# Performance work log

Hardware: AMD Instinct MI355X
Metric: run time of the kernel (lower is better)

Reference implementation:

```python
import jax, jax.numpy as jnp
import numpy as np

B, T, HE, L, HD = 512, 512, 512, 64, 512

def setup_inputs() -> dict:
    key = jax.random.key(0)
    ks = jax.random.split(key, 16)
    def w(k, shape):
        return jax.random.normal(k, shape, dtype=jnp.float32) * 0.05
    z32 = lambda n: jnp.zeros((n,), jnp.float32)
    return {
        "input_tensor": jax.random.normal(ks[0], (B, T, 1), dtype=jnp.float32),
        # encoder LSTMCell (keras gate order i, f, g, o)
        "enc_W": w(ks[1], (1, 4 * HE)),
        "enc_U": w(ks[2], (HE, 4 * HE)),
        "enc_b": z32(4 * HE),
        # encoder mu / std heads
        "emu_W": w(ks[3], (HE, L)), "emu_b": z32(L),
        "estd_W": w(ks[4], (HE, L)), "estd_b": z32(L),
        # decoder first-state dense (tanh)
        "dfs_W": w(ks[5], (L, HD)), "dfs_b": z32(HD),
        # decoder LSTMCell
        "dec_W": w(ks[6], (L, 4 * HD)),
        "dec_U": w(ks[7], (HD, 4 * HD)),
        "dec_b": z32(4 * HD),
        # decoder mu / std heads (Dense(1))
        "dmu_W": w(ks[8], (HD, 1)), "dmu_b": z32(1),
        "dstd_W": w(ks[9], (HD, 1)), "dstd_b": z32(1),
    }

def _lstm_update(gates, c):
    i, f, g, o = jnp.split(gates, 4, axis=-1)
    c_new = jax.nn.sigmoid(f) * c + jax.nn.sigmoid(i) * jnp.tanh(g)
    h_new = jax.nn.sigmoid(o) * jnp.tanh(c_new)
    return h_new, c_new

def reference(input_tensor, enc_W, enc_U, enc_b, emu_W, emu_b, estd_W, estd_b,
              dfs_W, dfs_b, dec_W, dec_U, dec_b, dmu_W, dmu_b, dstd_W, dstd_b):
    x = input_tensor
    Bn, Tn = x.shape[0], x.shape[1]
    He = enc_U.shape[0]

    # ---- encoder: LSTM over time, keep final h ----
    def enc_step(carry, xt):
        h, c = carry
        gates = xt @ enc_W + h @ enc_U + enc_b
        return _lstm_update(gates, c), None
    h0 = jnp.zeros((Bn, He), x.dtype)
    (hT, _), _ = jax.lax.scan(enc_step, (h0, h0), jnp.swapaxes(x, 0, 1))

    mu_enc = hT @ emu_W + emu_b                       # [B, L]
    sigma_enc = jax.nn.softplus(hT @ estd_W + estd_b)  # [B, L]
    z = mu_enc  # call() uses reparam=False -> latent returns mu

    # ---- decoder: LSTM fed constant z each step ----
    hd = jnp.tanh(z @ dfs_W + dfs_b)                  # [B, HD]
    cd = jnp.zeros_like(hd)
    zin = z @ dec_W + dec_b                           # input projection constant over t
    def dec_step(carry, _):
        h, c = carry
        h_new, c_new = _lstm_update(zin + h @ dec_U, c)
        mu = h_new @ dmu_W + dmu_b                    # [B, 1]
        sg = h_new @ dstd_W + dstd_b
        return (h_new, c_new), (mu, sg)
    _, (mus, sgs) = jax.lax.scan(dec_step, (hd, cd), None, length=Tn)

    mu_dec = jnp.swapaxes(mus, 0, 1)                  # [B, T, 1]
    sigma_dec = jax.nn.softplus(jnp.swapaxes(sgs, 0, 1))
    return (mu_dec, sigma_dec, mu_enc, sigma_enc)
```

## Files before the change

### kernel.cpp

```cpp
#include <hip/hip_runtime.h>


#define B_   512
#define T_   512
#define H_   512
#define NGR  32
#define WPG  8
#define RPG  16
#define UPW  64

typedef _Float16 f16;
typedef _Float16 f16x8 __attribute__((ext_vector_type(8)));
typedef float f32x16 __attribute__((ext_vector_type(16)));
typedef unsigned long long u64;
typedef unsigned int u32;

#define OFF_SG_DEC 262144
#define OFF_MU_ENC 524288
#define OFF_SG_ENC 557056

__device__ __forceinline__ float sigm_(float x) { return 1.f / (1.f + __expf(-x)); }
__device__ __forceinline__ float tanh_(float x) {
  float t = fabsf(x);
  float e = __expf(2.f * t);
  float r = 1.f - 2.f / (e + 1.f);
  return x < 0.f ? -r : r;
}
__device__ __forceinline__ float softplus_(float x) {
  return fmaxf(x, 0.f) + log1pf(__expf(-fabsf(x)));
}
__device__ __forceinline__ int fresh_(u64 w, u32 g) {
  return ((u32)(w >> 48) == g) & (((u32)(w >> 16) & 0xffffu) == g);
}
__device__ __forceinline__ u32 packh_(u64 w) {
  return (u32)(w & 0xffffu) | (((u32)(w >> 32) & 0xffffu) << 16);
}

__global__ void pack_U(const float* __restrict__ U, f16* __restrict__ Upk) {
  const int e = blockIdx.x * 256 + threadIdx.x;
  const int j = e & 7, lane = (e >> 3) & 63, ks = (e >> 9) & 31;
  const int w = (e >> 14) & 7, wg = (e >> 17) & 7;
  const int ccol = lane & 31, khalf = lane >> 5;
  const int uu = ccol >> 2, gate = ccol & 3;
  const int k = ks * 16 + khalf * 8 + j;
  const int gcol = gate * 512 + wg * UPW + w * 8 + uu;
  Upk[e] = (f16)U[k * 2048 + gcol];
}

template <int IS_DEC>
__global__ void __launch_bounds__(512, 1)
lstm_rec(const f16* __restrict__ Upk,
         const float* __restrict__ xin,
         const float* __restrict__ wa,
         const float* __restrict__ wb,
         u32* __restrict__ hbuf,
         float* __restrict__ accmu,
         float* __restrict__ accsg) {
  const int bid = blockIdx.x;
  const int wg = (bid >> 3) & 7;
  const int g = (bid & 7) * 4 + (bid >> 6);
  const int tid = threadIdx.x;
  const int wave = tid >> 6, lane = tid & 63;
  const int R0 = g * RPG;
  const int U0 = wg * UPW;
  const u32 GB = IS_DEC ? 0x8000u : 0u;

  const int ccol = lane & 31, khalf = lane >> 5;
  f16x8 Breg[32];
#pragma unroll
  for (int ks = 0; ks < 32; ++ks) {
    const f16* p = Upk + (((wg * 8 + wave) * 32 + ks) << 9) + lane * 8;
    asm volatile("global_load_dwordx4 %0, %1, off\n\ts_waitcnt vmcnt(0)"
                 : "=v"(Breg[ks]) : "v"(p));
  }

  const int row = tid >> 4;
  const int q = (tid & 15) * 4;
  float addv[16], xw[16];
  if (tid < 256) {
#pragma unroll
    for (int m = 0; m < 4; ++m) {
#pragma unroll
      for (int gt = 0; gt < 4; ++gt) {
        const int col = gt * 512 + U0 + q + m;
        if (IS_DEC) {
          addv[m * 4 + gt] = xin[(R0 + row) * 2048 + col];
          xw[m * 4 + gt] = 0.f;
        } else {
          addv[m * 4 + gt] = wb[col];
          xw[m * 4 + gt] = wa[col];
        }
      }
    }
  }
  float wmu[8], wsg[8];
  if (IS_DEC) {
#pragma unroll
    for (int j = 0; j < 8; ++j) {
      wmu[j] = wa[lane * 8 + j];
      wsg[j] = wb[lane * 8 + j];
    }
  }

  float cst[4] = {0.f, 0.f, 0.f, 0.f};

  __shared__ __align__(16) f16 hstage[2][RPG * 536];
  __shared__ float gatesLds[RPG * 260];
  __shared__ float xl[RPG * 516];

  if (!IS_DEC) {
#pragma unroll
    for (int i = 0; i < 16; ++i) {
      const int idx = tid + i * 512;
      const int r = idx >> 9, c2 = idx & 511;
      xl[r * 516 + c2] = xin[(R0 + r) * T_ + c2];
    }
    __syncthreads();
  }

  int srow[8], scol[8], gidx[8];
#pragma unroll
  for (int i = 0; i < 8; ++i) {
    const int w = tid + i * 512;
    srow[i] = w >> 8; scol[i] = w & 255;
    gidx[i] = (R0 + srow[i]) * 256 + scol[i];
  }
  const u64* hb64 = (const u64*)hbuf;
  const int hrow = lane & 15;

  u64 wr[8];
#pragma unroll
  for (int i = 0; i < 8; ++i)
    wr[i] = __hip_atomic_load(hb64 + gidx[i], __ATOMIC_RELAXED,
                              __HIP_MEMORY_SCOPE_AGENT);
  asm volatile("" ::: "memory");

  for (int t = 0; t < T_; ++t) {
    const int b0 = (t & 1) * 131072;
    const int b1 = ((t + 1) & 1) * 131072;
    const int c1 = ((t + 1) & 1) * 262144;
    const u32 gr = GB + (u32)t, gn = gr + 1u;

    for (;;) {
      int f = 1;
#pragma unroll
      for (int i = 0; i < 8; ++i) f &= fresh_(wr[i], gr);
      if (f) break;
#pragma unroll
      for (int i = 0; i < 8; ++i)
        wr[i] = __hip_atomic_load(hb64 + b0 + gidx[i], __ATOMIC_RELAXED,
                                  __HIP_MEMORY_SCOPE_AGENT);
    }
    f16* const sb = hstage[t & 1];
#pragma unroll
    for (int i = 0; i < 8; ++i)
      *(u32*)&sb[srow[i] * 536 + scol[i] * 2] = packh_(wr[i]);
    __syncthreads();

    f32x16 acc;
#pragma unroll
    for (int j = 0; j < 16; ++j) acc[j] = 0.f;
#pragma unroll
    for (int ks = 0; ks < 32; ++ks) {
      f16x8 a = *(const f16x8*)&sb[hrow * 536 + ks * 16 + khalf * 8];
      acc = __builtin_amdgcn_mfma_f32_32x32x16_f16(a, Breg[ks], acc, 0, 0, 0);
    }
#pragma unroll
    for (int r = 0; r < 8; ++r) {
      const int orow = (r & 3) + 8 * (r >> 2) + 4 * khalf;
      gatesLds[orow * 260 + wave * 32 + ccol] = acc[r];
    }
    __syncthreads();

    if (tid < 256) {
      float xv = 0.f;
      if (!IS_DEC) xv = xl[row * 516 + t];
      float hn[4];
#pragma unroll
      for (int m = 0; m < 4; ++m) {
        float ga[4];
#pragma unroll
        for (int gt = 0; gt < 4; ++gt) {
          float v = gatesLds[row * 260 + (q + m) * 4 + gt] + addv[m * 4 + gt];
          if (!IS_DEC) v += xv * xw[m * 4 + gt];
          ga[gt] = v;
        }
        const float iv = sigm_(ga[0]);
        const float fv = sigm_(ga[1]);
        const float gv = tanh_(ga[2]);
        const float ov = sigm_(ga[3]);
        const float cn = fv * cst[m] + iv * gv;
        cst[m] = cn;
        hn[m] = ov * tanh_(cn);
      }
      union { f16 h; unsigned short u; } hc0, hc1, hc2, hc3;
      hc0.h = (f16)hn[0]; hc1.h = (f16)hn[1];
      hc2.h = (f16)hn[2]; hc3.h = (f16)hn[3];
      const u64 tg = (u64)gn << 16;
      const u64 w0 = (tg | hc0.u) | (((tg | hc1.u)) << 32);
      const u64 w1 = (tg | hc2.u) | (((tg | hc3.u)) << 32);
      u64* hdst = (u64*)(hbuf + c1 + (R0 + row) * 512 + U0 + q);
      __hip_atomic_store(hdst, w0, __ATOMIC_RELAXED, __HIP_MEMORY_SCOPE_AGENT);
      __hip_atomic_store(hdst + 1, w1, __ATOMIC_RELAXED, __HIP_MEMORY_SCOPE_AGENT);
    }

#pragma unroll
    for (int i = 0; i < 8; ++i)
      wr[i] = __hip_atomic_load(hb64 + b1 + gidx[i], __ATOMIC_RELAXED,
                                __HIP_MEMORY_SCOPE_AGENT);
    asm volatile("" ::: "memory");

    if (IS_DEC && t >= 1 && wave < 2) {
      const int hr = 2 * wg + wave;
      const f16x8 hv = *(const f16x8*)&sb[hr * 536 + lane * 8];
      float smu = 0.f, ssg = 0.f;
#pragma unroll
      for (int j = 0; j < 8; ++j) {
        const float hq = (float)hv[j];
        smu += hq * wmu[j]; ssg += hq * wsg[j];
      }
#pragma unroll
      for (int o = 32; o; o >>= 1) {
        smu += __shfl_xor(smu, o); ssg += __shfl_xor(ssg, o);
      }
      if (lane == 0) {
        accmu[(R0 + hr) * 512 + (t - 1)] = smu;
        accsg[(R0 + hr) * 512 + (t - 1)] = ssg;
      }
    }
  }
}

__global__ void dec_tail(const u32* __restrict__ hbuf, const float* __restrict__ dmuW,
                         const float* __restrict__ dstdW, float* __restrict__ accmu,
                         float* __restrict__ accsg) {
  const int r = blockIdx.x, lane = threadIdx.x;
  float smu = 0.f, ssg = 0.f;
#pragma unroll
  for (int j = 0; j < 8; ++j) {
    union { unsigned short u; f16 h; } c;
    c.u = (unsigned short)(hbuf[r * 512 + lane * 8 + j] & 0xffffu);
    const float hq = (float)c.h;
    smu += hq * dmuW[lane * 8 + j];
    ssg += hq * dstdW[lane * 8 + j];
  }
#pragma unroll
  for (int o = 32; o; o >>= 1) {
    smu += __shfl_xor(smu, o); ssg += __shfl_xor(ssg, o);
  }
  if (lane == 0) {
    accmu[r * 512 + 511] = smu;
    accsg[r * 512 + 511] = ssg;
  }
}

__global__ void enc_heads(const u32* __restrict__ h0, const float* __restrict__ emuW,
                          const float* __restrict__ emub, const float* __restrict__ estdW,
                          const float* __restrict__ estdb, float* __restrict__ out,
                          float* __restrict__ z) {
  const int b = blockIdx.x, tid = threadIdx.x;
  __shared__ float hrow[512];
  for (int k = tid; k < 512; k += 128) {
    union { unsigned short u; f16 h; } c;
    c.u = (unsigned short)(h0[b * 512 + k] & 0xffffu);
    hrow[k] = (float)c.h;
  }
  __syncthreads();
  const int head = tid >> 6, l = tid & 63;
  const float* W = head ? estdW : emuW;
  float a = 0.f;
#pragma unroll 8
  for (int k = 0; k < 512; ++k) a += hrow[k] * W[k * 64 + l];
  if (head == 0) {
    const float v = a + emub[l];
    out[OFF_MU_ENC + b * 64 + l] = v;
    z[b * 64 + l] = v;
  } else {
    out[OFF_SG_ENC + b * 64 + l] = softplus_(a + estdb[l]);
  }
}

__global__ void dec_prep(const float* __restrict__ z, const float* __restrict__ dfsW,
                         const float* __restrict__ dfsb, const float* __restrict__ decW,
                         const float* __restrict__ decb, u32* __restrict__ hbuf,
                         float* __restrict__ zin) {
  const int b = blockIdx.x, tid = threadIdx.x;
  __shared__ float zl[64];
  if (tid < 64) zl[tid] = z[b * 64 + tid];
  __syncthreads();
  for (int c = tid; c < 512; c += 256) {
    float a = dfsb[c];
#pragma unroll
    for (int l = 0; l < 64; ++l) a += zl[l] * dfsW[l * 512 + c];
    union { f16 h; unsigned short u; } hc; hc.h = (f16)tanh_(a);
    hbuf[b * 512 + c] = (0x8000u << 16) | (u32)hc.u;
  }
  for (int c = tid; c < 2048; c += 256) {
    float a = decb[c];
#pragma unroll
    for (int l = 0; l < 64; ++l) a += zl[l] * decW[l * 2048 + c];
    zin[b * 2048 + c] = a;
  }
}

__global__ void finalize_k(const float* __restrict__ accmu, const float* __restrict__ accsg,
                           const float* __restrict__ dmub, const float* __restrict__ dstdb,
                           float* __restrict__ out) {
  const int i = blockIdx.x * 256 + threadIdx.x;
  out[i] = accmu[i] + dmub[0];
  out[OFF_SG_DEC + i] = softplus_(accsg[i] + dstdb[0]);
}

extern "C" void kernel_launch(void* const* d_in, const int* in_sizes, int n_in,
                              void* d_out, int out_size, void* d_ws, size_t ws_size,
                              hipStream_t stream) {
  (void)in_sizes; (void)n_in; (void)out_size; (void)ws_size;
  const float* x     = (const float*)d_in[0];
  const float* encW  = (const float*)d_in[1];
  const float* encU  = (const float*)d_in[2];
  const float* encb  = (const float*)d_in[3];
  const float* emuW  = (const float*)d_in[4];
  const float* emub  = (const float*)d_in[5];
  const float* estdW = (const float*)d_in[6];
  const float* estdb = (const float*)d_in[7];
  const float* dfsW  = (const float*)d_in[8];
  const float* dfsb  = (const float*)d_in[9];
  const float* decW  = (const float*)d_in[10];
  const float* decU  = (const float*)d_in[11];
  const float* decb  = (const float*)d_in[12];
  const float* dmuW  = (const float*)d_in[13];
  const float* dmub  = (const float*)d_in[14];
  const float* dstdW = (const float*)d_in[15];
  const float* dstdb = (const float*)d_in[16];

  char* ws = (char*)d_ws;
  u32*   hbuf  = (u32*)(ws + 0);
  float* accmu = (float*)(ws + (2u << 20));
  float* accsg = (float*)(ws + (3u << 20));
  f16*   UpkE  = (f16*)(ws + (4u << 20));
  float* zin   = (float*)(ws + (4u << 20));
  f16*   UpkD  = (f16*)(ws + (8u << 20));
  float* z     = (float*)(ws + (10u << 20));
  float* out   = (float*)d_out;

  hipMemsetAsync(d_ws, 0, 2u << 20, stream);

  hipLaunchKernelGGL(pack_U, dim3(4096), dim3(256), 0, stream, encU, UpkE);
  hipLaunchKernelGGL(pack_U, dim3(4096), dim3(256), 0, stream, decU, UpkD);

  hipLaunchKernelGGL((lstm_rec<0>), dim3(256), dim3(512), 0, stream,
                     UpkE, x, encW, encb, hbuf, (float*)nullptr, (float*)nullptr);
  hipLaunchKernelGGL(enc_heads, dim3(512), dim3(128), 0, stream,
                     hbuf, emuW, emub, estdW, estdb, out, z);
  hipLaunchKernelGGL(dec_prep, dim3(512), dim3(256), 0, stream,
                     z, dfsW, dfsb, decW, decb, hbuf, zin);
  hipLaunchKernelGGL((lstm_rec<1>), dim3(256), dim3(512), 0, stream,
                     UpkD, zin, dmuW, dstdW, hbuf, accmu, accsg);
  hipLaunchKernelGGL(dec_tail, dim3(512), dim3(64), 0, stream,
                     hbuf, dmuW, dstdW, accmu, accsg);
  hipLaunchKernelGGL(finalize_k, dim3(1024), dim3(256), 0, stream,
                     accmu, accsg, dmub, dstdb, out);
}
```

Baseline: 4.896 ms.

## Drop prefetch and double-buffered stage; fuse decoder heads via atomics

The recurrent kernel stops prefetching the next step's hidden state and drops the double-buffered LDS stage. It now loads and spin-waits per element each step into a single stage buffer. The decoder output heads are computed from each thread's own new h values, reduced over 16 lanes and atomically added into the accumulators, which removes the dec_tail kernel and the wave-level head pass. The accumulators are zeroed by a larger memset. This removes the separate head pass and the tail launch, but gives up load latency overlap and adds atomic traffic, and the single stage buffer may race with slower waves still reading it.

Result: slower. 5.433 ms (+11.0%).

```diff
diff --git a/kernel.cpp b/kernel.cpp
--- a/kernel.cpp
+++ b/kernel.cpp
@@ -76,7 +76,7 @@
 
   const int row = tid >> 4;
   const int q = (tid & 15) * 4;
-  float addv[16], xw[16];
+  float addv[16], xw[16], dmur[4], dstdr[4];
   if (tid < 256) {
 #pragma unroll
     for (int m = 0; m < 4; ++m) {
@@ -91,20 +91,19 @@
           xw[m * 4 + gt] = wa[col];
         }
       }
-    }
-  }
-  float wmu[8], wsg[8];
-  if (IS_DEC) {
-#pragma unroll
-    for (int j = 0; j < 8; ++j) {
-      wmu[j] = wa[lane * 8 + j];
-      wsg[j] = wb[lane * 8 + j];
+      if (IS_DEC) {
+        dmur[m] = wa[U0 + q + m];
+        dstdr[m] = wb[U0 + q + m];
+      } else {
+        dmur[m] = 0.f;
+        dstdr[m] = 0.f;
+      }
     }
   }
 
   float cst[4] = {0.f, 0.f, 0.f, 0.f};
 
-  __shared__ __align__(16) f16 hstage[2][RPG * 536];
+  __shared__ __align__(16) f16 hstage[RPG * 536];
   __shared__ float gatesLds[RPG * 260];
   __shared__ float xl[RPG * 516];
 
@@ -128,33 +127,24 @@
   const u64* hb64 = (const u64*)hbuf;
   const int hrow = lane & 15;
 
-  u64 wr[8];
-#pragma unroll
-  for (int i = 0; i < 8; ++i)
-    wr[i] = __hip_atomic_load(hb64 + gidx[i], __ATOMIC_RELAXED,
-                              __HIP_MEMORY_SCOPE_AGENT);
-  asm volatile("" ::: "memory");
-
   for (int t = 0; t < T_; ++t) {
     const int b0 = (t & 1) * 131072;
-    const int b1 = ((t + 1) & 1) * 131072;
     const int c1 = ((t + 1) & 1) * 262144;
     const u32 gr = GB + (u32)t, gn = gr + 1u;
 
-    for (;;) {
-      int f = 1;
-#pragma unroll
-      for (int i = 0; i < 8; ++i) f &= fresh_(wr[i], gr);
-      if (f) break;
-#pragma unroll
-      for (int i = 0; i < 8; ++i)
-        wr[i] = __hip_atomic_load(hb64 + b0 + gidx[i], __ATOMIC_RELAXED,
-                                  __HIP_MEMORY_SCOPE_AGENT);
-    }
-    f16* const sb = hstage[t & 1];
+    u64 v[8];
 #pragma unroll
     for (int i = 0; i < 8; ++i)
-      *(u32*)&sb[srow[i] * 536 + scol[i] * 2] = packh_(wr[i]);
+      v[i] = __hip_atomic_load(hb64 + b0 + gidx[i], __ATOMIC_RELAXED,
+                               __HIP_MEMORY_SCOPE_AGENT);
+#pragma unroll
+    for (int i = 0; i < 8; ++i) {
+      u64 w = v[i];
+      while (!fresh_(w, gr))
+        w = __hip_atomic_load(hb64 + b0 + gidx[i], __ATOMIC_RELAXED,
+                              __HIP_MEMORY_SCOPE_AGENT);
+      *(u32*)&hstage[srow[i] * 536 + scol[i] * 2] = packh_(w);
+    }
     __syncthreads();
 
     f32x16 acc;
@@ -162,7 +152,7 @@
     for (int j = 0; j < 16; ++j) acc[j] = 0.f;
 #pragma unroll
     for (int ks = 0; ks < 32; ++ks) {
-      f16x8 a = *(const f16x8*)&sb[hrow * 536 + ks * 16 + khalf * 8];
+      f16x8 a = *(const f16x8*)&hstage[hrow * 536 + ks * 16 + khalf * 8];
       acc = __builtin_amdgcn_mfma_f32_32x32x16_f16(a, Breg[ks], acc, 0, 0, 0);
     }
 #pragma unroll
@@ -181,9 +171,9 @@
         float ga[4];
 #pragma unroll
         for (int gt = 0; gt < 4; ++gt) {
-          float v = gatesLds[row * 260 + (q + m) * 4 + gt] + addv[m * 4 + gt];
-          if (!IS_DEC) v += xv * xw[m * 4 + gt];
-          ga[gt] = v;
+          float vg = gatesLds[row * 260 + (q + m) * 4 + gt] + addv[m * 4 + gt];
+          if (!IS_DEC) vg += xv * xw[m * 4 + gt];
+          ga[gt] = vg;
         }
         const float iv = sigm_(ga[0]);
         const float fv = sigm_(ga[1]);
@@ -193,64 +183,34 @@
         cst[m] = cn;
         hn[m] = ov * tanh_(cn);
       }
-      union { f16 h; unsigned short u; } hc0, hc1, hc2, hc3;
-      hc0.h = (f16)hn[0]; hc1.h = (f16)hn[1];
-      hc2.h = (f16)hn[2]; hc3.h = (f16)hn[3];
+      union { f16 h; unsigned short u; } h0_, h1_, h2_, h3_;
+      h0_.h = (f16)hn[0]; h1_.h = (f16)hn[1];
+      h2_.h = (f16)hn[2]; h3_.h = (f16)hn[3];
       const u64 tg = (u64)gn << 16;
-      const u64 w0 = (tg | hc0.u) | (((tg | hc1.u)) << 32);
-      const u64 w1 = (tg | hc2.u) | (((tg | hc3.u)) << 32);
+      const u64 w0 = (tg | h0_.u) | ((tg | h1_.u) << 32);
+      const u64 w1 = (tg | h2_.u) | ((tg | h3_.u) << 32);
       u64* hdst = (u64*)(hbuf + c1 + (R0 + row) * 512 + U0 + q);
       __hip_atomic_store(hdst, w0, __ATOMIC_RELAXED, __HIP_MEMORY_SCOPE_AGENT);
       __hip_atomic_store(hdst + 1, w1, __ATOMIC_RELAXED, __HIP_MEMORY_SCOPE_AGENT);
-    }
-
-#pragma unroll
-    for (int i = 0; i < 8; ++i)
-      wr[i] = __hip_atomic_load(hb64 + b1 + gidx[i], __ATOMIC_RELAXED,
-                                __HIP_MEMORY_SCOPE_AGENT);
-    asm volatile("" ::: "memory");
-
-    if (IS_DEC && t >= 1 && wave < 2) {
-      const int hr = 2 * wg + wave;
-      const f16x8 hv = *(const f16x8*)&sb[hr * 536 + lane * 8];
-      float smu = 0.f, ssg = 0.f;
-#pragma unroll
-      for (int j = 0; j < 8; ++j) {
-        const float hq = (float)hv[j];
-        smu += hq * wmu[j]; ssg += hq * wsg[j];
+
+      if (IS_DEC) {
+        float pmu = 0.f, psg = 0.f;
+#pragma unroll
+        for (int m = 0; m < 4; ++m) {
+          pmu += (float)((f16)hn[m]) * dmur[m];
+          psg += (float)((f16)hn[m]) * dstdr[m];
+        }
+#pragma unroll
+        for (int o = 1; o < 16; o <<= 1) {
+          pmu += __shfl_xor(pmu, o);
+          psg += __shfl_xor(psg, o);
+        }
+        if ((tid & 15) == 0) {
+          unsafeAtomicAdd(&accmu[(R0 + row) * T_ + t], pmu);
+          unsafeAtomicAdd(&accsg[(R0 + row) * T_ + t], psg);
+        }
       }
-#pragma unroll
-      for (int o = 32; o; o >>= 1) {
-        smu += __shfl_xor(smu, o); ssg += __shfl_xor(ssg, o);
-      }
-      if (lane == 0) {
-        accmu[(R0 + hr) * 512 + (t - 1)] = smu;
-        accsg[(R0 + hr) * 512 + (t - 1)] = ssg;
-      }
-    }
-  }
-}
-
-__global__ void dec_tail(const u32* __restrict__ hbuf, const float* __restrict__ dmuW,
-                         const float* __restrict__ dstdW, float* __restrict__ accmu,
-                         float* __restrict__ accsg) {
-  const int r = blockIdx.x, lane = threadIdx.x;
-  float smu = 0.f, ssg = 0.f;
-#pragma unroll
-  for (int j = 0; j < 8; ++j) {
-    union { unsigned short u; f16 h; } c;
-    c.u = (unsigned short)(hbuf[r * 512 + lane * 8 + j] & 0xffffu);
-    const float hq = (float)c.h;
-    smu += hq * dmuW[lane * 8 + j];
-    ssg += hq * dstdW[lane * 8 + j];
-  }
-#pragma unroll
-  for (int o = 32; o; o >>= 1) {
-    smu += __shfl_xor(smu, o); ssg += __shfl_xor(ssg, o);
-  }
-  if (lane == 0) {
-    accmu[r * 512 + 511] = smu;
-    accsg[r * 512 + 511] = ssg;
+    }
   }
 }
 
@@ -343,7 +303,7 @@
   float* z     = (float*)(ws + (10u << 20));
   float* out   = (float*)d_out;
 
-  hipMemsetAsync(d_ws, 0, 2u << 20, stream);
+  hipMemsetAsync(d_ws, 0, 4u << 20, stream);
 
   hipLaunchKernelGGL(pack_U, dim3(4096), dim3(256), 0, stream, encU, UpkE);
   hipLaunchKernelGGL(pack_U, dim3(4096), dim3(256), 0, stream, decU, UpkD);
@@ -356,8 +316,6 @@
                      z, dfsW, dfsb, decW, decb, hbuf, zin);
   hipLaunchKernelGGL((lstm_rec<1>), dim3(256), dim3(512), 0, stream,
                      UpkD, zin, dmuW, dstdW, hbuf, accmu, accsg);
-  hipLaunchKernelGGL(dec_tail, dim3(512), dim3(64), 0, stream,
-                     hbuf, dmuW, dstdW, accmu, accsg);
   hipLaunchKernelGGL(finalize_k, dim3(1024), dim3(256), 0, stream,
                      accmu, accsg, dmub, dstdb, out);
 }
```
